# Kernel optimization log

Hardware: AMD Instinct MI355X
Metric: run time of the kernel (lower is better)

## Reference

```python
import jax, jax.numpy as jnp
import numpy as np

# Grid / problem sizes (full-res grid for sp_tensor_1; sp_tensor_2 lives on the half-res grid
# and its indices are multiplied by 2 in forward, so they land on even full-res coords).
B, Z, Y, X = 2, 21, 400, 352
Z2, Y2, X2 = 11, 200, 176
N1, N2 = 160000, 60000
CIN, COUT = 64, 128
EPS = 1e-3  # BatchNorm eps


def _build_rulebook():
    """Precompute the SubMConv3d rulebook (spconv builds this once per indice_key).
    Returns padded gather/scatter index arrays for the 26 non-center taps and N.
    Padding uses index N (a dummy zero row / dropped output row)."""
    rng = np.random.default_rng(0)
    # sp_tensor_2: unique voxels on half-res grid, coords scaled by 2 (as done in forward)
    lin2 = rng.choice(B * Z2 * Y2 * X2, size=N2, replace=False)
    b2 = lin2 // (Z2 * Y2 * X2); r = lin2 % (Z2 * Y2 * X2)
    z2 = r // (Y2 * X2); r = r % (Y2 * X2); y2 = r // X2; x2 = r % X2
    c2 = np.stack([b2, 2 * z2, 2 * y2, 2 * x2], 1).astype(np.int64)
    key2 = ((c2[:, 0] * Z + c2[:, 1]) * Y + c2[:, 2]) * X + c2[:, 3]
    # sp_tensor_1: unique voxels on full-res grid, disjoint from scaled sp2 voxels
    lin1 = rng.choice(B * Z * Y * X, size=N1 + 20000, replace=False)
    lin1 = lin1[~np.isin(lin1, key2)][:N1].astype(np.int64)
    b1 = lin1 // (Z * Y * X); r = lin1 % (Z * Y * X)
    z1 = r // (Y * X); r = r % (Y * X); y1 = r // X; x1 = r % X
    c1 = np.stack([b1, z1, y1, x1], 1)
    coords = np.concatenate([c1, c2], 0)  # [N,4] -- sp1 rows first, matching feature concat
    N = coords.shape[0]
    keys = ((coords[:, 0] * Z + coords[:, 1]) * Y + coords[:, 2]) * X + coords[:, 3]
    order = np.argsort(keys); skeys = keys[order]
    gathers, scatters = [], []
    for dz in (-1, 0, 1):
        for dy in (-1, 0, 1):
            for dx in (-1, 0, 1):
                if dz == 0 and dy == 0 and dx == 0:
                    continue  # center tap handled as a dense identity-indexed GEMM
                q = coords[:, 1:] + np.array([dz, dy, dx])
                valid = (q >= 0).all(1) & (q[:, 0] < Z) & (q[:, 1] < Y) & (q[:, 2] < X)
                qk = ((coords[:, 0] * Z + q[:, 0]) * Y + q[:, 1]) * X + q[:, 2]
                pos = np.clip(np.searchsorted(skeys, qk), 0, N - 1)
                hit = valid & (skeys[pos] == qk)
                gathers.append(order[pos[hit]])
                scatters.append(np.nonzero(hit)[0])
    Pmax = max(len(g) for g in gathers)
    G = np.full((26, Pmax), N, np.int32)
    S = np.full((26, Pmax), N, np.int32)
    for i, (g, s) in enumerate(zip(gathers, scatters)):
        G[i, :len(g)] = g
        S[i, :len(s)] = s
    return G, S, N


def setup_inputs() -> dict:
    G, S, N = _build_rulebook()
    k1, k2, k3, k4 = jax.random.split(jax.random.key(0), 4)
    return {
        "features1": jax.random.normal(k1, (N1, CIN), jnp.float32),
        "features2": jax.random.normal(k2, (N - N1, CIN), jnp.float32),
        "weight": jax.random.normal(k3, (27, CIN, COUT), jnp.float32) * (1.0 / np.sqrt(27 * CIN)),
        "bias": jax.random.normal(k4, (COUT,), jnp.float32) * 0.01,
        "gamma": jnp.ones((COUT,), jnp.float32),
        "beta": jnp.zeros((COUT,), jnp.float32),
        "gather_idx": jnp.asarray(G),
        "scatter_idx": jnp.asarray(S),
    }


def reference(features1, features2, weight, bias, gamma, beta, gather_idx, scatter_idx):
    # forward(): concat features of both sparse tensors along the voxel axis
    feats = jnp.concatenate([features1, features2], axis=0)  # [N, Cin]
    N = feats.shape[0]
    # SubMConv3d via gather-GEMM-scatter over the precomputed rulebook.
    # Center tap (kernel index 13): every output voxel pairs with itself -> dense GEMM.
    out = feats @ weight[13] + bias  # [N, Cout]
    # dummy row N absorbs padded rulebook entries
    out = jnp.concatenate([out, jnp.zeros((1, out.shape[1]), out.dtype)], axis=0)
    feats_pad = jnp.concatenate([feats, jnp.zeros((1, feats.shape[1]), feats.dtype)], axis=0)
    taps = [k for k in range(27) if k != 13]
    for i, k in enumerate(taps):
        msg = feats_pad[gather_idx[i]] @ weight[k]  # [Pmax, Cout]
        out = out.at[scatter_idx[i]].add(msg)
    out = out[:N]
    # BatchNorm1d (training mode: batch statistics, biased variance) + ReLU
    mean = jnp.mean(out, axis=0)
    var = jnp.var(out, axis=0)
    out = (out - mean) * jax.lax.rsqrt(var + EPS) * gamma + beta
    return jax.nn.relu(out)
```

## Files before the change

kernel.cpp:

```cpp
#include <hip/hip_runtime.h>

#define EPS 1e-3f

typedef __attribute__((ext_vector_type(8))) short bf8_t;
typedef __attribute__((ext_vector_type(4))) float f32x4;

static __device__ __forceinline__ unsigned f2bf_pack(float a, float b) {
  union { float f; unsigned u; } ca, cb;
  ca.f = a; cb.f = b;
  unsigned ra = (ca.u + 0x7FFFu + ((ca.u >> 16) & 1u)) >> 16;
  unsigned rb = (cb.u + 0x7FFFu + ((cb.u >> 16) & 1u)) >> 16;
  return ra | (rb << 16);
}
static __device__ __forceinline__ unsigned short f2bf1(float x) {
  union { float f; unsigned u; } c; c.f = x;
  return (unsigned short)((c.u + 0x7FFFu + ((c.u >> 16) & 1u)) >> 16);
}
static __device__ __forceinline__ float bf2f(unsigned bits16) {
  union { unsigned u; float f; } c;
  c.u = bits16 << 16;
  return c.f;
}


__global__ __launch_bounds__(256) void to_bf16(
    const float* __restrict__ f1, const float* __restrict__ f2,
    unsigned short* __restrict__ fbuf, int N1, int N) {
  int idx = blockIdx.x * 256 + threadIdx.x;
  if (idx >= (N + 1) * 8) return;
  int row = idx >> 3, seg = idx & 7;
  uint4 o = make_uint4(0, 0, 0, 0);
  if (row < N) {
    const float* src = (row < N1) ? (f1 + (size_t)row * 64)
                                  : (f2 + (size_t)(row - N1) * 64);
    float4 v0 = *(const float4*)(src + seg * 8);
    float4 v1 = *(const float4*)(src + seg * 8 + 4);
    o.x = f2bf_pack(v0.x, v0.y); o.y = f2bf_pack(v0.z, v0.w);
    o.z = f2bf_pack(v1.x, v1.y); o.w = f2bf_pack(v1.z, v1.w);
  }
  *(uint4*)(fbuf + (size_t)idx * 8) = o;
}

__global__ __launch_bounds__(256) void wconv(
    const float* __restrict__ W, unsigned short* __restrict__ Wb) {
  int idx = blockIdx.x * 256 + threadIdx.x;
  int k = idx & 63, n = (idx >> 6) & 127, t = idx >> 13;
  Wb[idx] = f2bf1(W[((size_t)t * 64 + k) * 128 + n]);
}

__global__ __launch_bounds__(256) void count_slots(
    const int* __restrict__ S, unsigned char* __restrict__ SL,
    int* __restrict__ cnt, int N, int pm) {
  const int p = blockIdx.x * 256 + threadIdx.x;
  const int i = blockIdx.y;
  if (p >= pm) return;
  const int idx = i * pm + p;
  const int s = S[idx];
  if (s < N) SL[idx] = (unsigned char)atomicAdd(&cnt[s], 1);
}

__global__ __launch_bounds__(256) void prefix_base(
    const int* __restrict__ cnt, int2* __restrict__ BC,
    int* __restrict__ gtot, int N) {
  const int t = threadIdx.x;
  const int j0 = blockIdx.x * 1024 + t * 4;
  int c0 = 0, c1 = 0, c2 = 0, c3 = 0;
  if (j0 + 3 < N) {
    int4 c = *(const int4*)(cnt + j0);
    c0 = c.x; c1 = c.y; c2 = c.z; c3 = c.w;
  } else {
    if (j0 < N) c0 = cnt[j0];
    if (j0 + 1 < N) c1 = cnt[j0 + 1];
    if (j0 + 2 < N) c2 = cnt[j0 + 2];
  }
  const int tsum = c0 + c1 + c2 + c3;
  int incl = tsum;
#pragma unroll
  for (int off = 1; off < 64; off <<= 1) {
    int u = __shfl_up(incl, off, 64);
    if ((t & 63) >= off) incl += u;
  }
  __shared__ int wsum[4];
  if ((t & 63) == 63) wsum[t >> 6] = incl;
  __syncthreads();
  if (t == 0) {
    int w0 = wsum[0], w1 = wsum[1], w2 = wsum[2], w3 = wsum[3];
    int gb = atomicAdd(gtot, w0 + w1 + w2 + w3);
    wsum[0] = gb; wsum[1] = gb + w0;
    wsum[2] = gb + w0 + w1; wsum[3] = gb + w0 + w1 + w2;
  }
  __syncthreads();
  const int excl = wsum[t >> 6] + incl - tsum;
  if (j0 < N) BC[j0] = make_int2(excl, c0);
  if (j0 + 1 < N) BC[j0 + 1] = make_int2(excl + c0, c1);
  if (j0 + 2 < N) BC[j0 + 2] = make_int2(excl + c0 + c1, c2);
  if (j0 + 3 < N) BC[j0 + 3] = make_int2(excl + c0 + c1 + c2, c3);
}

__global__ __launch_bounds__(256) void center_mfma(
    const unsigned short* __restrict__ fbuf,
    const unsigned short* __restrict__ Wb13,
    const float* __restrict__ bias,
    unsigned short* __restrict__ outb, int N) {
  __shared__ unsigned short A[128 * 64];
  const int tid = threadIdx.x;
  const int row0 = blockIdx.x * 128;

#pragma unroll
  for (int it = 0; it < 4; ++it) {
    int flat = it * 256 + tid;
    int r = flat >> 3, qs = flat & 7;
    int g = row0 + r; if (g >= N) g = N;
    uint4 v = *(const uint4*)(fbuf + (size_t)g * 64 + qs * 8);
    int rt = r >> 4, m = r & 15, c = qs >> 2, qq = qs & 3;
    *(uint4*)(A + ((rt * 2 + c) * 64 + qq * 16 + m) * 8) = v;
  }
  __syncthreads();

  const int wave = tid >> 6, lane = tid & 63;
  const int ncol = lane & 15, q2 = lane >> 4;
  bf8_t Bf[2][2];
  float bs[2];
#pragma unroll
  for (int ct = 0; ct < 2; ++ct) {
    int col = wave * 32 + ct * 16 + ncol;
    bs[ct] = bias[col];
#pragma unroll
    for (int c = 0; c < 2; ++c)
      Bf[ct][c] = *(const bf8_t*)(Wb13 + (size_t)col * 64 + c * 32 + q2 * 8);
  }
  f32x4 acc[8][2];
#pragma unroll
  for (int rt = 0; rt < 8; ++rt)
#pragma unroll
    for (int ct = 0; ct < 2; ++ct) acc[rt][ct] = (f32x4){0.f, 0.f, 0.f, 0.f};

#pragma unroll
  for (int rt = 0; rt < 8; ++rt) {
    bf8_t a0 = *(const bf8_t*)(A + ((rt * 2 + 0) * 64 + lane) * 8);
    bf8_t a1 = *(const bf8_t*)(A + ((rt * 2 + 1) * 64 + lane) * 8);
#pragma unroll
    for (int ct = 0; ct < 2; ++ct) {
      acc[rt][ct] = __builtin_amdgcn_mfma_f32_16x16x32_bf16(a0, Bf[ct][0], acc[rt][ct], 0, 0, 0);
      acc[rt][ct] = __builtin_amdgcn_mfma_f32_16x16x32_bf16(a1, Bf[ct][1], acc[rt][ct], 0, 0, 0);
    }
  }

#pragma unroll
  for (int rt = 0; rt < 8; ++rt)
#pragma unroll
    for (int ct = 0; ct < 2; ++ct) {
      int col = wave * 32 + ct * 16 + ncol;
#pragma unroll
      for (int e = 0; e < 4; ++e) {
        int row = row0 + rt * 16 + q2 * 4 + e;
        if (row < N)
          outb[(size_t)row * 128 + col] = f2bf1(acc[rt][ct][e] + bs[ct]);
      }
    }
}

__global__ __launch_bounds__(256) void msg_mfma_c(
    const unsigned short* __restrict__ fbuf,
    const unsigned short* __restrict__ Wb,
    const int* __restrict__ G, const int* __restrict__ S,
    const int2* __restrict__ BC, const unsigned char* __restrict__ SL,
    unsigned short* __restrict__ compact, int N, int pm) {
  const int tap = blockIdx.y;
  const int ktap = tap + (tap >= 13 ? 1 : 0);
  const unsigned short* Wt = Wb + (size_t)ktap * 128 * 64;
  const int* Gi = G + (size_t)tap * pm;
  const int* Si = S + (size_t)tap * pm;
  const int p0 = blockIdx.x * 128;
  if (Gi[p0] >= N) return;

  __shared__ unsigned short A[128 * 64];
  __shared__ int g_lds[128];
  __shared__ int d_lds[128];
  const int tid = threadIdx.x;
  if (tid < 128) {
    int p = p0 + tid;
    int g = N, d = -1;
    if (p < pm) {
      g = Gi[p];
      int s = Si[p];
      if (s < N) d = BC[s].x + (int)SL[(size_t)tap * pm + p];
    }
    g_lds[tid] = g;
    d_lds[tid] = d;
  }
  __syncthreads();

#pragma unroll
  for (int it = 0; it < 4; ++it) {
    int flat = it * 256 + tid;
    int r = flat >> 3, qs = flat & 7;
    int g = g_lds[r];
    uint4 v = *(const uint4*)(fbuf + (size_t)g * 64 + qs * 8);
    int rt = r >> 4, m = r & 15, c = qs >> 2, qq = qs & 3;
    *(uint4*)(A + ((rt * 2 + c) * 64 + qq * 16 + m) * 8) = v;
  }
  __syncthreads();

  const int wave = tid >> 6, lane = tid & 63;
  const int ncol = lane & 15, q2 = lane >> 4;
  bf8_t Bf[2][2];
#pragma unroll
  for (int ct = 0; ct < 2; ++ct) {
    int col = wave * 32 + ct * 16 + ncol;
#pragma unroll
    for (int c = 0; c < 2; ++c)
      Bf[ct][c] = *(const bf8_t*)(Wt + (size_t)col * 64 + c * 32 + q2 * 8);
  }
  f32x4 acc[8][2];
#pragma unroll
  for (int rt = 0; rt < 8; ++rt)
#pragma unroll
    for (int ct = 0; ct < 2; ++ct) acc[rt][ct] = (f32x4){0.f, 0.f, 0.f, 0.f};

#pragma unroll
  for (int rt = 0; rt < 8; ++rt) {
    bf8_t a0 = *(const bf8_t*)(A + ((rt * 2 + 0) * 64 + lane) * 8);
    bf8_t a1 = *(const bf8_t*)(A + ((rt * 2 + 1) * 64 + lane) * 8);
#pragma unroll
    for (int ct = 0; ct < 2; ++ct) {
      acc[rt][ct] = __builtin_amdgcn_mfma_f32_16x16x32_bf16(a0, Bf[ct][0], acc[rt][ct], 0, 0, 0);
      acc[rt][ct] = __builtin_amdgcn_mfma_f32_16x16x32_bf16(a1, Bf[ct][1], acc[rt][ct], 0, 0, 0);
    }
  }

#pragma unroll
  for (int rt = 0; rt < 8; ++rt) {
    int dl[4];
#pragma unroll
    for (int e = 0; e < 4; ++e) dl[e] = d_lds[rt * 16 + q2 * 4 + e];
#pragma unroll
    for (int ct = 0; ct < 2; ++ct) {
      int col = wave * 32 + ct * 16 + ncol;
#pragma unroll
      for (int e = 0; e < 4; ++e)
        if (dl[e] >= 0)
          compact[(size_t)dl[e] * 128 + col] = f2bf1(acc[rt][ct][e]);
    }
  }
}

__global__ __launch_bounds__(256) void combine_c(
    unsigned short* __restrict__ outb, const int2* __restrict__ BC,
    const unsigned short* __restrict__ compact, float* __restrict__ ws,
    int N) {
  const int tid = threadIdx.x;
  const int grp = tid >> 5, l = tid & 31;
  float4 s = make_float4(0.f, 0.f, 0.f, 0.f);
  float4 q = make_float4(0.f, 0.f, 0.f, 0.f);

  for (int j = blockIdx.x * 8 + grp; j < N; j += gridDim.x * 8) {
    int2 bc = BC[j];
    uint2 ov = ((const uint2*)(outb + (size_t)j * 128))[l];
    float4 v;
    v.x = bf2f(ov.x & 0xffffu); v.y = bf2f(ov.x >> 16);
    v.z = bf2f(ov.y & 0xffffu); v.w = bf2f(ov.y >> 16);
    for (int k = 0; k < bc.y; ++k) {
      uint2 mv = ((const uint2*)(compact + (size_t)(bc.x + k) * 128))[l];
      v.x += bf2f(mv.x & 0xffffu); v.y += bf2f(mv.x >> 16);
      v.z += bf2f(mv.y & 0xffffu); v.w += bf2f(mv.y >> 16);
    }
    if (bc.y) {
      uint2 pk;
      pk.x = f2bf_pack(v.x, v.y); pk.y = f2bf_pack(v.z, v.w);
      ((uint2*)(outb + (size_t)j * 128))[l] = pk;
    }
    s.x += v.x; s.y += v.y; s.z += v.z; s.w += v.w;
    q.x += v.x * v.x; q.y += v.y * v.y; q.z += v.z * v.z; q.w += v.w * v.w;
  }

  __shared__ float red[8 * 32 * 9];
  float* my = red + (grp * 32 + l) * 9;
  my[0] = s.x; my[1] = s.y; my[2] = s.z; my[3] = s.w;
  my[4] = q.x; my[5] = q.y; my[6] = q.z; my[7] = q.w;
  __syncthreads();
  {
    int c4 = tid & 31, jj = tid >> 5;
    float v = 0.f;
#pragma unroll
    for (int g = 0; g < 8; ++g) v += red[(g * 32 + c4) * 9 + jj];
    int col = c4 * 4 + (jj & 3);
    unsafeAtomicAdd(&ws[(jj >> 2) * 4096 + col * 16], v);
  }
}

__global__ __launch_bounds__(256) void norm_b(
    const unsigned short* __restrict__ outb, float* __restrict__ out,
    const float* __restrict__ ws, const float* __restrict__ gamma,
    const float* __restrict__ beta, int total8, float invN) {
  const int tid0 = blockIdx.x * 256 + threadIdx.x;
  const int c0 = (tid0 & 15) * 8;
  float sc[8], sh[8];
#pragma unroll
  for (int k = 0; k < 8; ++k) {
    float m = ws[(c0 + k) * 16] * invN;
    float var = ws[4096 + (c0 + k) * 16] * invN - m * m;
    sc[k] = gamma[c0 + k] * rsqrtf(var + EPS);
    sh[k] = beta[c0 + k] - m * sc[k];
  }
  for (int idx = tid0; idx < total8; idx += gridDim.x * 256) {
    uint4 v = *(const uint4*)(outb + (size_t)idx * 8);
    float f0 = bf2f(v.x & 0xffffu), f1 = bf2f(v.x >> 16);
    float f2 = bf2f(v.y & 0xffffu), f3 = bf2f(v.y >> 16);
    float f4 = bf2f(v.z & 0xffffu), f5 = bf2f(v.z >> 16);
    float f6 = bf2f(v.w & 0xffffu), f7 = bf2f(v.w >> 16);
    float4 o0, o1;
    o0.x = fmaxf(f0 * sc[0] + sh[0], 0.f);
    o0.y = fmaxf(f1 * sc[1] + sh[1], 0.f);
    o0.z = fmaxf(f2 * sc[2] + sh[2], 0.f);
    o0.w = fmaxf(f3 * sc[3] + sh[3], 0.f);
    o1.x = fmaxf(f4 * sc[4] + sh[4], 0.f);
    o1.y = fmaxf(f5 * sc[5] + sh[5], 0.f);
    o1.z = fmaxf(f6 * sc[6] + sh[6], 0.f);
    o1.w = fmaxf(f7 * sc[7] + sh[7], 0.f);
    *(float4*)(out + (size_t)idx * 8) = o0;
    *(float4*)(out + (size_t)idx * 8 + 4) = o1;
  }
}


__global__ __launch_bounds__(256) void scatter_R(
    const int* __restrict__ S, int* __restrict__ R, int N, int pm) {
  const int p = blockIdx.x * 256 + threadIdx.x;
  const int i = blockIdx.y;
  if (p >= pm) return;
  const int idx = i * pm + p;
  const int s = S[idx];
  if (s < N) R[(size_t)s * 26 + i] = idx;
}

__global__ __launch_bounds__(256) void center_gemm(
    const float* __restrict__ f1, const float* __restrict__ f2,
    const float* __restrict__ W, const float* __restrict__ bias,
    float* __restrict__ out, int N, int N1) {
  __shared__ float fLDS[128 * 65];
  __shared__ float wLDS[32 * 128];
  const int tid = threadIdx.x;
  const int tx = tid & 15, ty = tid >> 4;
  const int row0 = blockIdx.x * 128;

  for (int k = 0; k < 8; ++k) {
    int flat4 = tid + k * 256;
    int row = flat4 >> 4, c4 = flat4 & 15;
    int grow = row0 + row;
    float4 v = make_float4(0.f, 0.f, 0.f, 0.f);
    if (grow < N) {
      const float* src = (grow < N1) ? (f1 + (size_t)grow * 64)
                                     : (f2 + (size_t)(grow - N1) * 64);
      v = *(const float4*)(src + c4 * 4);
    }
    int l = row * 65 + c4 * 4;
    fLDS[l + 0] = v.x; fLDS[l + 1] = v.y; fLDS[l + 2] = v.z; fLDS[l + 3] = v.w;
  }
  float acc[8][8];
#pragma unroll
  for (int r = 0; r < 8; ++r)
#pragma unroll
    for (int j = 0; j < 8; ++j) acc[r][j] = 0.f;
  for (int kk = 0; kk < 64; kk += 32) {
    __syncthreads();
    for (int k = 0; k < 4; ++k) {
      int flat4 = tid + k * 256;
      int c = flat4 >> 5, col4 = flat4 & 31;
      float4 v = *(const float4*)(W + (size_t)(kk + c) * 128 + col4 * 4);
      *(float4*)(wLDS + c * 128 + col4 * 4) = v;
    }
    __syncthreads();
#pragma unroll 4
    for (int c = 0; c < 32; ++c) {
      float a[8];
#pragma unroll
      for (int r = 0; r < 8; ++r) a[r] = fLDS[(ty * 8 + r) * 65 + kk + c];
      float4 b0 = *(const float4*)(wLDS + c * 128 + tx * 8);
      float4 b1 = *(const float4*)(wLDS + c * 128 + tx * 8 + 4);
      float b[8] = {b0.x, b0.y, b0.z, b0.w, b1.x, b1.y, b1.z, b1.w};
#pragma unroll
      for (int r = 0; r < 8; ++r)
#pragma unroll
        for (int j = 0; j < 8; ++j) acc[r][j] += a[r] * b[j];
    }
  }
  float4 bi0 = *(const float4*)(bias + tx * 8);
  float4 bi1 = *(const float4*)(bias + tx * 8 + 4);
#pragma unroll
  for (int r = 0; r < 8; ++r) {
    int grow = row0 + ty * 8 + r;
    if (grow < N) {
      float4 o0 = make_float4(acc[r][0] + bi0.x, acc[r][1] + bi0.y,
                              acc[r][2] + bi0.z, acc[r][3] + bi0.w);
      float4 o1 = make_float4(acc[r][4] + bi1.x, acc[r][5] + bi1.y,
                              acc[r][6] + bi1.z, acc[r][7] + bi1.w);
      float* dst = out + (size_t)grow * 128 + tx * 8;
      *(float4*)dst = o0;
      *(float4*)(dst + 4) = o1;
    }
  }
}

__global__ __launch_bounds__(256) void msg_gemm_buf(
    const float* __restrict__ f1, const float* __restrict__ f2,
    const float* __restrict__ W27, const int* __restrict__ G,
    const int* __restrict__ S, unsigned short* __restrict__ msgbuf,
    int N, int N1, int pm) {
  const int i = blockIdx.y;
  const int ktap = i + (i >= 13 ? 1 : 0);
  const float* W = W27 + (size_t)ktap * 64 * 128;
  const int* Gi = G + (size_t)i * pm;
  const int* Si = S + (size_t)i * pm;
  const int p0 = blockIdx.x * 128;
  if (Si[p0] >= N) return;
  __shared__ float fLDS[128 * 65];
  __shared__ float wLDS[32 * 128];
  const int tid = threadIdx.x;
  const int tx = tid & 15, ty = tid >> 4;
  for (int k = 0; k < 8; ++k) {
    int flat4 = tid + k * 256;
    int row = flat4 >> 4, c4 = flat4 & 15;
    int p = p0 + row;
    float4 v = make_float4(0.f, 0.f, 0.f, 0.f);
    if (p < pm) {
      int g = Gi[p];
      if (g < N) {
        const float* src = (g < N1) ? (f1 + (size_t)g * 64)
                                    : (f2 + (size_t)(g - N1) * 64);
        v = *(const float4*)(src + c4 * 4);
      }
    }
    int l = row * 65 + c4 * 4;
    fLDS[l + 0] = v.x; fLDS[l + 1] = v.y; fLDS[l + 2] = v.z; fLDS[l + 3] = v.w;
  }
  float acc[8][8];
#pragma unroll
  for (int r = 0; r < 8; ++r)
#pragma unroll
    for (int j = 0; j < 8; ++j) acc[r][j] = 0.f;
// ... 82 lines not shown
    __syncthreads();
#pragma unroll 4
    for (int c = 0; c < 32; ++c) {
      float a[8];
#pragma unroll
      for (int r = 0; r < 8; ++r) a[r] = fLDS[(ty * 8 + r) * 65 + kk + c];
      float4 b0 = *(const float4*)(wLDS + c * 128 + tx * 8);
      float4 b1 = *(const float4*)(wLDS + c * 128 + tx * 8 + 4);
      float b[8] = {b0.x, b0.y, b0.z, b0.w, b1.x, b1.y, b1.z, b1.w};
#pragma unroll
      for (int r = 0; r < 8; ++r)
#pragma unroll
        for (int j = 0; j < 8; ++j) acc[r][j] += a[r] * b[j];
    }
  }
#pragma unroll
  for (int r = 0; r < 8; ++r) {
    int p = p0 + ty * 8 + r;
    if (p < pm) {
      int s = Si[p];
      if (s < N) {
        float* dst = out + (size_t)s * 128 + tx * 8;
#pragma unroll
        for (int j = 0; j < 8; ++j) unsafeAtomicAdd(dst + j, acc[r][j]);
      }
    }
  }
}

__global__ __launch_bounds__(256) void combine_stats(
    float* __restrict__ out, const int* __restrict__ R,
    const unsigned short* __restrict__ msgbuf, float* __restrict__ ws,
    int N) {
  const int tid = threadIdx.x;
  const int grp = tid >> 5, l = tid & 31;
  const int base = tid & 32;
  float4 s = make_float4(0.f, 0.f, 0.f, 0.f);
  float4 q = make_float4(0.f, 0.f, 0.f, 0.f);
  for (int j = blockIdx.x * 8 + grp; j < N; j += gridDim.x * 8) {
    float4 v = ((const float4*)(out + (size_t)j * 128))[l];
    int r = (l < 26) ? R[(size_t)j * 26 + l] : -1;
    unsigned long long bal = __ballot(r >= 0);
    unsigned mym = (unsigned)((bal >> base) & 0x3FFFFFFull);
    const bool any = (mym != 0);
    while (mym) {
      int b = __builtin_ctz(mym);
      mym &= mym - 1;
      int ptr = __shfl(r, base + b, 64);
      uint2 mv = ((const uint2*)(msgbuf + (size_t)ptr * 128))[l];
      v.x += bf2f(mv.x & 0xffffu);
      v.y += bf2f(mv.x >> 16);
      v.z += bf2f(mv.y & 0xffffu);
      v.w += bf2f(mv.y >> 16);
    }
    if (any) ((float4*)(out + (size_t)j * 128))[l] = v;
    s.x += v.x; s.y += v.y; s.z += v.z; s.w += v.w;
    q.x += v.x * v.x; q.y += v.y * v.y; q.z += v.z * v.z; q.w += v.w * v.w;
  }
  __shared__ float red[8 * 32 * 8];
  float* my = red + (grp * 32 + l) * 8;
  my[0] = s.x; my[1] = s.y; my[2] = s.z; my[3] = s.w;
  my[4] = q.x; my[5] = q.y; my[6] = q.z; my[7] = q.w;
  __syncthreads();
  {
    int c4 = tid & 31, j = tid >> 5;
    float v = 0.f;
#pragma unroll
    for (int g = 0; g < 8; ++g) v += red[(g * 32 + c4) * 8 + j];
    int col = c4 * 4 + (j & 3);
    unsafeAtomicAdd(&ws[col + (j >> 2) * 128], v);
  }
}

__global__ __launch_bounds__(256) void stats_kernel(
    const float* __restrict__ out, float* __restrict__ ws, int total4) {
  const int tid = threadIdx.x;
  float4 s = make_float4(0.f, 0.f, 0.f, 0.f);
  float4 q = make_float4(0.f, 0.f, 0.f, 0.f);
  const float4* o4 = (const float4*)out;
  for (int idx = blockIdx.x * 256 + tid; idx < total4; idx += gridDim.x * 256) {
    float4 v = o4[idx];
    s.x += v.x; s.y += v.y; s.z += v.z; s.w += v.w;
    q.x += v.x * v.x; q.y += v.y * v.y; q.z += v.z * v.z; q.w += v.w * v.w;
  }
  __shared__ float red[8 * 32 * 8];
  const int col4 = tid & 31, grpq = tid >> 5;
  float* my = red + (grpq * 32 + col4) * 8;
  my[0] = s.x; my[1] = s.y; my[2] = s.z; my[3] = s.w;
  my[4] = q.x; my[5] = q.y; my[6] = q.z; my[7] = q.w;
  __syncthreads();
  {
    int c4 = tid & 31, j = tid >> 5;
    float v = 0.f;
#pragma unroll
    for (int g = 0; g < 8; ++g) v += red[(g * 32 + c4) * 8 + j];
    int col = c4 * 4 + (j & 3);
    unsafeAtomicAdd(&ws[col + (j >> 2) * 128], v);
  }
}

__global__ __launch_bounds__(256) void norm_kernel(
    float* __restrict__ out, const float* __restrict__ ws,
    const float* __restrict__ gamma, const float* __restrict__ beta,
    int total4, float invN) {
  const int tid = threadIdx.x;
  const int c4 = tid & 31;
  float4 s = ((const float4*)ws)[c4];
  float4 q = ((const float4*)ws)[32 + c4];
  float4 g = ((const float4*)gamma)[c4];
  float4 b = ((const float4*)beta)[c4];
  float m0 = s.x * invN, m1 = s.y * invN, m2 = s.z * invN, m3 = s.w * invN;
  float sc0 = g.x * rsqrtf(q.x * invN - m0 * m0 + EPS);
  float sc1 = g.y * rsqrtf(q.y * invN - m1 * m1 + EPS);
  float sc2 = g.z * rsqrtf(q.z * invN - m2 * m2 + EPS);
  float sc3 = g.w * rsqrtf(q.w * invN - m3 * m3 + EPS);
  float sh0 = b.x - m0 * sc0, sh1 = b.y - m1 * sc1;
  float sh2 = b.z - m2 * sc2, sh3 = b.w - m3 * sc3;
  float4* o4 = (float4*)out;
  for (int idx = blockIdx.x * 256 + tid; idx < total4; idx += gridDim.x * 256) {
    float4 v = o4[idx];
    v.x = fmaxf(v.x * sc0 + sh0, 0.f);
    v.y = fmaxf(v.y * sc1 + sh1, 0.f);
    v.z = fmaxf(v.z * sc2 + sh2, 0.f);
    v.w = fmaxf(v.w * sc3 + sh3, 0.f);
    o4[idx] = v;
  }
}

extern "C" void kernel_launch(void* const* d_in, const int* in_sizes, int n_in,
                              void* d_out, int out_size, void* d_ws, size_t ws_size,
                              hipStream_t stream) {
  const float* f1 = (const float*)d_in[0];
  const float* f2 = (const float*)d_in[1];
  const float* W = (const float*)d_in[2];
  const float* bias = (const float*)d_in[3];
  const float* gamma = (const float*)d_in[4];
  const float* beta = (const float*)d_in[5];
  const int* G = (const int*)d_in[6];
  const int* S = (const int*)d_in[7];
  const int N1 = in_sizes[0] / 64;
  const int N2 = in_sizes[1] / 64;
  const int N = N1 + N2;
  const int pm = in_sizes[6] / 26;
  float* out = (float*)d_out;
  float* ws = (float*)d_ws;

  const size_t AL = 255;
  const size_t offC = 32768;
  const size_t Cb = (size_t)N * 4;
  const size_t offBC = (offC + Cb + AL) & ~AL;
  const size_t BCb = (size_t)N * 8;
  const size_t offSL = (offBC + BCb + AL) & ~AL;
  const size_t SLb = (size_t)26 * pm;
  const size_t offF = (offSL + SLb + AL) & ~AL;
  const size_t Fb = (size_t)(N + 1) * 64 * 2;
  const size_t offW = (offF + Fb + AL) & ~AL;
  const size_t Wbyt = (size_t)27 * 128 * 64 * 2;
  const size_t offM = (offW + Wbyt + AL) & ~AL;
  const size_t Mb = (size_t)26 * pm * 128 * 2;
  const size_t offO = (offM + Mb + AL) & ~AL;
  const size_t Ob = (size_t)N * 128 * 2;
  const bool full = ws_size >= offO + Ob;

  const size_t Rb = (size_t)N * 26 * 4;
  const size_t offR2 = 1024;
  const size_t offM2 = (offR2 + Rb + AL) & ~AL;
  const bool fast2 = ws_size >= offM2 + Mb;

  if (full) {
    int* cnt = (int*)((char*)d_ws + offC);
    int2* BC = (int2*)((char*)d_ws + offBC);
    unsigned char* SLp = (unsigned char*)((char*)d_ws + offSL);
    unsigned short* fbuf = (unsigned short*)((char*)d_ws + offF);
    unsigned short* Wb = (unsigned short*)((char*)d_ws + offW);
    unsigned short* compact = (unsigned short*)((char*)d_ws + offM);
    unsigned short* outb = (unsigned short*)((char*)d_ws + offO);
    int* gtot = (int*)((char*)d_ws + 28672);

    (void)hipMemsetAsync(ws, 0, 32768, stream);
    (void)hipMemsetAsync(cnt, 0, Cb, stream);
    to_bf16<<<((N + 1) * 8 + 255) / 256, 256, 0, stream>>>(f1, f2, fbuf, N1, N);
    wconv<<<(27 * 128 * 64) / 256, 256, 0, stream>>>(W, Wb);
    count_slots<<<dim3((pm + 255) / 256, 26), 256, 0, stream>>>(S, SLp, cnt, N, pm);
    prefix_base<<<(N + 1023) / 1024, 256, 0, stream>>>(cnt, BC, gtot, N);

    center_mfma<<<(N + 127) / 128, 256, 0, stream>>>(
        fbuf, Wb + (size_t)13 * 128 * 64, bias, outb, N);
    msg_mfma_c<<<dim3((pm + 127) / 128, 26), 256, 0, stream>>>(
        fbuf, Wb, G, S, BC, SLp, compact, N, pm);

    combine_c<<<2048, 256, 0, stream>>>(outb, BC, compact, ws, N);
    norm_b<<<2048, 256, 0, stream>>>(outb, out, ws, gamma, beta, N * 16,
                                     1.0f / N);
  } else if (fast2) {
    int* R = (int*)((char*)d_ws + offR2);
    unsigned short* msgbuf = (unsigned short*)((char*)d_ws + offM2);
    (void)hipMemsetAsync(ws, 0, 256 * sizeof(float), stream);
    (void)hipMemsetAsync(R, 0xFF, Rb, stream);
    center_gemm<<<(N + 127) / 128, 256, 0, stream>>>(
        f1, f2, W + (size_t)13 * 64 * 128, bias, out, N, N1);
    scatter_R<<<dim3((pm + 255) / 256, 26), 256, 0, stream>>>(S, R, N, pm);
    msg_gemm_buf<<<dim3((pm + 127) / 128, 26), 256, 0, stream>>>(
        f1, f2, W, G, S, msgbuf, N, N1, pm);
    combine_stats<<<1024, 256, 0, stream>>>(out, R, msgbuf, ws, N);
    norm_kernel<<<2048, 256, 0, stream>>>(out, ws, gamma, beta, N * 32,
                                          1.0f / N);
  } else {
    (void)hipMemsetAsync(ws, 0, 256 * sizeof(float), stream);
    center_gemm<<<(N + 127) / 128, 256, 0, stream>>>(
        f1, f2, W + (size_t)13 * 64 * 128, bias, out, N, N1);
    msg_gemm<<<dim3((pm + 127) / 128, 26), 256, 0, stream>>>(
        f1, f2, W, G, S, out, N, N1, pm);
    stats_kernel<<<1024, 256, 0, stream>>>(out, ws, N * 32);
    norm_kernel<<<2048, 256, 0, stream>>>(out, ws, gamma, beta, N * 32,
                                          1.0f / N);
  }
}
```

Baseline: 334.1 us.

## Fuse bf16 conversion into GEMMs and center GEMM into combine

Removes the separate fp32-to-bf16 feature buffer, so the message and center GEMM kernels read fp32 features directly and convert while staging into LDS. The center GEMM is fused with the combine/statistics pass, so output rows are written once after adding the compacted messages. Weight conversion and slot counting are merged into one launch, and the two memsets become one. This cuts launches and a full round trip of the bf16 feature and output buffers. In exchange, gathers now read twice as many bytes of fp32 per row, and the combine's compact reads are per-column scalar loads rather than vectorised.

```diff
diff --git a/kernel.cpp b/kernel.cpp
--- a/kernel.cpp
+++ b/kernel.cpp
@@ -23,40 +23,24 @@
 }
 
 
-__global__ __launch_bounds__(256) void to_bf16(
-    const float* __restrict__ f1, const float* __restrict__ f2,
-    unsigned short* __restrict__ fbuf, int N1, int N) {
-  int idx = blockIdx.x * 256 + threadIdx.x;
-  if (idx >= (N + 1) * 8) return;
-  int row = idx >> 3, seg = idx & 7;
-  uint4 o = make_uint4(0, 0, 0, 0);
-  if (row < N) {
-    const float* src = (row < N1) ? (f1 + (size_t)row * 64)
-                                  : (f2 + (size_t)(row - N1) * 64);
-    float4 v0 = *(const float4*)(src + seg * 8);
-    float4 v1 = *(const float4*)(src + seg * 8 + 4);
-    o.x = f2bf_pack(v0.x, v0.y); o.y = f2bf_pack(v0.z, v0.w);
-    o.z = f2bf_pack(v1.x, v1.y); o.w = f2bf_pack(v1.z, v1.w);
-  }
-  *(uint4*)(fbuf + (size_t)idx * 8) = o;
-}
-
-__global__ __launch_bounds__(256) void wconv(
-    const float* __restrict__ W, unsigned short* __restrict__ Wb) {
-  int idx = blockIdx.x * 256 + threadIdx.x;
-  int k = idx & 63, n = (idx >> 6) & 127, t = idx >> 13;
-  Wb[idx] = f2bf1(W[((size_t)t * 64 + k) * 128 + n]);
-}
-
-__global__ __launch_bounds__(256) void count_slots(
+__global__ __launch_bounds__(256) void prep(
+    const float* __restrict__ W, unsigned short* __restrict__ Wb,
     const int* __restrict__ S, unsigned char* __restrict__ SL,
-    int* __restrict__ cnt, int N, int pm) {
-  const int p = blockIdx.x * 256 + threadIdx.x;
-  const int i = blockIdx.y;
-  if (p >= pm) return;
-  const int idx = i * pm + p;
-  const int s = S[idx];
-  if (s < N) SL[idx] = (unsigned char)atomicAdd(&cnt[s], 1);
+    int* __restrict__ cnt, int N, int pm, int wblocks, int cpb) {
+  const int bid = blockIdx.x;
+  if (bid < wblocks) {
+    int idx = bid * 256 + threadIdx.x;
+    int k = idx & 63, n = (idx >> 6) & 127, t = idx >> 13;
+    Wb[idx] = f2bf1(W[((size_t)t * 64 + k) * 128 + n]);
+  } else {
+    int b = bid - wblocks;
+    int tap = b / cpb;
+    int p = (b - tap * cpb) * 256 + threadIdx.x;
+    if (p >= pm) return;
+    const int idx = tap * pm + p;
+    const int s = S[idx];
+    if (s < N) SL[idx] = (unsigned char)atomicAdd(&cnt[s], 1);
+  }
 }
 
 __global__ __launch_bounds__(256) void prefix_base(
@@ -97,75 +81,12 @@
   if (j0 + 3 < N) BC[j0 + 3] = make_int2(excl + c0 + c1 + c2, c3);
 }
 
-__global__ __launch_bounds__(256) void center_mfma(
-    const unsigned short* __restrict__ fbuf,
-    const unsigned short* __restrict__ Wb13,
-    const float* __restrict__ bias,
-    unsigned short* __restrict__ outb, int N) {
-  __shared__ unsigned short A[128 * 64];
-  const int tid = threadIdx.x;
-  const int row0 = blockIdx.x * 128;
-
-#pragma unroll
-  for (int it = 0; it < 4; ++it) {
-    int flat = it * 256 + tid;
-    int r = flat >> 3, qs = flat & 7;
-    int g = row0 + r; if (g >= N) g = N;
-    uint4 v = *(const uint4*)(fbuf + (size_t)g * 64 + qs * 8);
-    int rt = r >> 4, m = r & 15, c = qs >> 2, qq = qs & 3;
-    *(uint4*)(A + ((rt * 2 + c) * 64 + qq * 16 + m) * 8) = v;
-  }
-  __syncthreads();
-
-  const int wave = tid >> 6, lane = tid & 63;
-  const int ncol = lane & 15, q2 = lane >> 4;
-  bf8_t Bf[2][2];
-  float bs[2];
-#pragma unroll
-  for (int ct = 0; ct < 2; ++ct) {
-    int col = wave * 32 + ct * 16 + ncol;
-    bs[ct] = bias[col];
-#pragma unroll
-    for (int c = 0; c < 2; ++c)
-      Bf[ct][c] = *(const bf8_t*)(Wb13 + (size_t)col * 64 + c * 32 + q2 * 8);
-  }
-  f32x4 acc[8][2];
-#pragma unroll
-  for (int rt = 0; rt < 8; ++rt)
-#pragma unroll
-    for (int ct = 0; ct < 2; ++ct) acc[rt][ct] = (f32x4){0.f, 0.f, 0.f, 0.f};
-
-#pragma unroll
-  for (int rt = 0; rt < 8; ++rt) {
-    bf8_t a0 = *(const bf8_t*)(A + ((rt * 2 + 0) * 64 + lane) * 8);
-    bf8_t a1 = *(const bf8_t*)(A + ((rt * 2 + 1) * 64 + lane) * 8);
-#pragma unroll
-    for (int ct = 0; ct < 2; ++ct) {
-      acc[rt][ct] = __builtin_amdgcn_mfma_f32_16x16x32_bf16(a0, Bf[ct][0], acc[rt][ct], 0, 0, 0);
-      acc[rt][ct] = __builtin_amdgcn_mfma_f32_16x16x32_bf16(a1, Bf[ct][1], acc[rt][ct], 0, 0, 0);
-    }
-  }
-
-#pragma unroll
-  for (int rt = 0; rt < 8; ++rt)
-#pragma unroll
-    for (int ct = 0; ct < 2; ++ct) {
-      int col = wave * 32 + ct * 16 + ncol;
-#pragma unroll
-      for (int e = 0; e < 4; ++e) {
-        int row = row0 + rt * 16 + q2 * 4 + e;
-        if (row < N)
-          outb[(size_t)row * 128 + col] = f2bf1(acc[rt][ct][e] + bs[ct]);
-      }
-    }
-}
-
 __global__ __launch_bounds__(256) void msg_mfma_c(
-    const unsigned short* __restrict__ fbuf,
+    const float* __restrict__ f1, const float* __restrict__ f2,
     const unsigned short* __restrict__ Wb,
     const int* __restrict__ G, const int* __restrict__ S,
     const int2* __restrict__ BC, const unsigned char* __restrict__ SL,
-    unsigned short* __restrict__ compact, int N, int pm) {
+    unsigned short* __restrict__ compact, int N, int N1, int pm) {
   const int tap = blockIdx.y;
   const int ktap = tap + (tap >= 13 ? 1 : 0);
   const unsigned short* Wt = Wb + (size_t)ktap * 128 * 64;
@@ -196,9 +117,17 @@
     int flat = it * 256 + tid;
     int r = flat >> 3, qs = flat & 7;
     int g = g_lds[r];
-    uint4 v = *(const uint4*)(fbuf + (size_t)g * 64 + qs * 8);
+    uint4 o = make_uint4(0, 0, 0, 0);
+    if (g < N) {
+      const float* src = (g < N1) ? (f1 + (size_t)g * 64)
+                                  : (f2 + (size_t)(g - N1) * 64);
+      float4 v0 = *(const float4*)(src + qs * 8);
+      float4 v1 = *(const float4*)(src + qs * 8 + 4);
+      o.x = f2bf_pack(v0.x, v0.y); o.y = f2bf_pack(v0.z, v0.w);
+      o.z = f2bf_pack(v1.x, v1.y); o.w = f2bf_pack(v1.z, v1.w);
+    }
     int rt = r >> 4, m = r & 15, c = qs >> 2, qq = qs & 3;
-    *(uint4*)(A + ((rt * 2 + c) * 64 + qq * 16 + m) * 8) = v;
+    *(uint4*)(A + ((rt * 2 + c) * 64 + qq * 16 + m) * 8) = o;
   }
   __syncthreads();
 
@@ -245,47 +174,108 @@
   }
 }
 
-__global__ __launch_bounds__(256) void combine_c(
-    unsigned short* __restrict__ outb, const int2* __restrict__ BC,
-    const unsigned short* __restrict__ compact, float* __restrict__ ws,
-    int N) {
+__global__ __launch_bounds__(256) void center_combine(
+    const float* __restrict__ f1, const float* __restrict__ f2,
+    const unsigned short* __restrict__ Wb13, const float* __restrict__ bias,
+    const int2* __restrict__ BC, const unsigned short* __restrict__ compact,
+    unsigned short* __restrict__ outb, float* __restrict__ ws,
+    int N, int N1) {
+  __shared__ unsigned short A[128 * 64];
+  __shared__ int2 bc_lds[128];
+  __shared__ float2 red2[128 * 4];
   const int tid = threadIdx.x;
-  const int grp = tid >> 5, l = tid & 31;
-  float4 s = make_float4(0.f, 0.f, 0.f, 0.f);
-  float4 q = make_float4(0.f, 0.f, 0.f, 0.f);
-
-  for (int j = blockIdx.x * 8 + grp; j < N; j += gridDim.x * 8) {
-    int2 bc = BC[j];
-    uint2 ov = ((const uint2*)(outb + (size_t)j * 128))[l];
-    float4 v;
-    v.x = bf2f(ov.x & 0xffffu); v.y = bf2f(ov.x >> 16);
-    v.z = bf2f(ov.y & 0xffffu); v.w = bf2f(ov.y >> 16);
-    for (int k = 0; k < bc.y; ++k) {
-      uint2 mv = ((const uint2*)(compact + (size_t)(bc.x + k) * 128))[l];
-      v.x += bf2f(mv.x & 0xffffu); v.y += bf2f(mv.x >> 16);
-      v.z += bf2f(mv.y & 0xffffu); v.w += bf2f(mv.y >> 16);
-    }
-    if (bc.y) {
-      uint2 pk;
-      pk.x = f2bf_pack(v.x, v.y); pk.y = f2bf_pack(v.z, v.w);
-      ((uint2*)(outb + (size_t)j * 128))[l] = pk;
-    }
-    s.x += v.x; s.y += v.y; s.z += v.z; s.w += v.w;
-    q.x += v.x * v.x; q.y += v.y * v.y; q.z += v.z * v.z; q.w += v.w * v.w;
-  }
-
-  __shared__ float red[8 * 32 * 9];
-  float* my = red + (grp * 32 + l) * 9;
-  my[0] = s.x; my[1] = s.y; my[2] = s.z; my[3] = s.w;
-  my[4] = q.x; my[5] = q.y; my[6] = q.z; my[7] = q.w;
+  const int row0 = blockIdx.x * 128;
+
+  if (tid < 128) {
+    int r = row0 + tid;
+    int2 bc = make_int2(0, 0);
+    if (r < N) bc = BC[r];
+    bc_lds[tid] = bc;
+  }
+
+#pragma unroll
+  for (int it = 0; it < 4; ++it) {
+    int flat = it * 256 + tid;
+    int r = flat >> 3, qs = flat & 7;
+    int g = row0 + r;
+    uint4 o = make_uint4(0, 0, 0, 0);
+    if (g < N) {
+      const float* src = (g < N1) ? (f1 + (size_t)g * 64)
+                                  : (f2 + (size_t)(g - N1) * 64);
+      float4 v0 = *(const float4*)(src + qs * 8);
+      float4 v1 = *(const float4*)(src + qs * 8 + 4);
+      o.x = f2bf_pack(v0.x, v0.y); o.y = f2bf_pack(v0.z, v0.w);
+      o.z = f2bf_pack(v1.x, v1.y); o.w = f2bf_pack(v1.z, v1.w);
+    }
+    int rt = r >> 4, m = r & 15, c = qs >> 2, qq = qs & 3;
+    *(uint4*)(A + ((rt * 2 + c) * 64 + qq * 16 + m) * 8) = o;
+  }
   __syncthreads();
-  {
-    int c4 = tid & 31, jj = tid >> 5;
-    float v = 0.f;
-#pragma unroll
-    for (int g = 0; g < 8; ++g) v += red[(g * 32 + c4) * 9 + jj];
-    int col = c4 * 4 + (jj & 3);
-    unsafeAtomicAdd(&ws[(jj >> 2) * 4096 + col * 16], v);
+
+  const int wave = tid >> 6, lane = tid & 63;
+  const int ncol = lane & 15, q2 = lane >> 4;
+  bf8_t Bf[2][2];
+  float bs[2];
+#pragma unroll
+  for (int ct = 0; ct < 2; ++ct) {
+    int col = wave * 32 + ct * 16 + ncol;
+    bs[ct] = bias[col];
+#pragma unroll
+    for (int c = 0; c < 2; ++c)
+      Bf[ct][c] = *(const bf8_t*)(Wb13 + (size_t)col * 64 + c * 32 + q2 * 8);
+  }
+  f32x4 acc[8][2];
+#pragma unroll
+  for (int rt = 0; rt < 8; ++rt)
+#pragma unroll
+    for (int ct = 0; ct < 2; ++ct) acc[rt][ct] = (f32x4){0.f, 0.f, 0.f, 0.f};
+
+#pragma unroll
+  for (int rt = 0; rt < 8; ++rt) {
+    bf8_t a0 = *(const bf8_t*)(A + ((rt * 2 + 0) * 64 + lane) * 8);
+    bf8_t a1 = *(const bf8_t*)(A + ((rt * 2 + 1) * 64 + lane) * 8);
+#pragma unroll
+    for (int ct = 0; ct < 2; ++ct) {
+      acc[rt][ct] = __builtin_amdgcn_mfma_f32_16x16x32_bf16(a0, Bf[ct][0], acc[rt][ct], 0, 0, 0);
+      acc[rt][ct] = __builtin_amdgcn_mfma_f32_16x16x32_bf16(a1, Bf[ct][1], acc[rt][ct], 0, 0, 0);
+    }
+  }
+
+  float sacc[2] = {0.f, 0.f}, qacc[2] = {0.f, 0.f};
+#pragma unroll
+  for (int rt = 0; rt < 8; ++rt) {
+    int2 bcv[4];
+#pragma unroll
+    for (int e = 0; e < 4; ++e) bcv[e] = bc_lds[rt * 16 + q2 * 4 + e];
+#pragma unroll
+    for (int ct = 0; ct < 2; ++ct) {
+      int col = wave * 32 + ct * 16 + ncol;
+#pragma unroll
+      for (int e = 0; e < 4; ++e) {
+        int row = row0 + rt * 16 + q2 * 4 + e;
+        if (row < N) {
+          float v = acc[rt][ct][e] + bs[ct];
+          for (int k = 0; k < bcv[e].y; ++k)
+            v += bf2f(compact[(size_t)(bcv[e].x + k) * 128 + col]);
+          outb[(size_t)row * 128 + col] = f2bf1(v);
+          sacc[ct] += v; qacc[ct] += v * v;
+        }
+      }
+    }
+  }
+#pragma unroll
+  for (int ct = 0; ct < 2; ++ct) {
+    int col = wave * 32 + ct * 16 + ncol;
+    red2[col * 4 + q2] = make_float2(sacc[ct], qacc[ct]);
+  }
+  __syncthreads();
+  if (tid < 128) {
+    float2 a0 = red2[tid * 4 + 0], a1 = red2[tid * 4 + 1];
+    float2 a2 = red2[tid * 4 + 2], a3 = red2[tid * 4 + 3];
+    float ssum = a0.x + a1.x + a2.x + a3.x;
+    float qsum = a0.y + a1.y + a2.y + a3.y;
+    unsafeAtomicAdd(&ws[tid * 16], ssum);
+    unsafeAtomicAdd(&ws[4096 + tid * 16], qsum);
   }
 }
 
@@ -674,9 +664,7 @@
   const size_t BCb = (size_t)N * 8;
   const size_t offSL = (offBC + BCb + AL) & ~AL;
   const size_t SLb = (size_t)26 * pm;
-  const size_t offF = (offSL + SLb + AL) & ~AL;
-  const size_t Fb = (size_t)(N + 1) * 64 * 2;
-  const size_t offW = (offF + Fb + AL) & ~AL;
+  const size_t offW = (offSL + SLb + AL) & ~AL;
   const size_t Wbyt = (size_t)27 * 128 * 64 * 2;
   const size_t offM = (offW + Wbyt + AL) & ~AL;
   const size_t Mb = (size_t)26 * pm * 128 * 2;
@@ -693,25 +681,23 @@
     int* cnt = (int*)((char*)d_ws + offC);
     int2* BC = (int2*)((char*)d_ws + offBC);
     unsigned char* SLp = (unsigned char*)((char*)d_ws + offSL);
-    unsigned short* fbuf = (unsigned short*)((char*)d_ws + offF);
     unsigned short* Wb = (unsigned short*)((char*)d_ws + offW);
     unsigned short* compact = (unsigned short*)((char*)d_ws + offM);
     unsigned short* outb = (unsigned short*)((char*)d_ws + offO);
     int* gtot = (int*)((char*)d_ws + 28672);
 
-    (void)hipMemsetAsync(ws, 0, 32768, stream);
-    (void)hipMemsetAsync(cnt, 0, Cb, stream);
-    to_bf16<<<((N + 1) * 8 + 255) / 256, 256, 0, stream>>>(f1, f2, fbuf, N1, N);
-    wconv<<<(27 * 128 * 64) / 256, 256, 0, stream>>>(W, Wb);
-    count_slots<<<dim3((pm + 255) / 256, 26), 256, 0, stream>>>(S, SLp, cnt, N, pm);
+    const int wblocks = (27 * 128 * 64) / 256;
+    const int cpb = (pm + 255) / 256;
+
+    (void)hipMemsetAsync(ws, 0, offC + Cb, stream);
+    prep<<<wblocks + 26 * cpb, 256, 0, stream>>>(W, Wb, S, SLp, cnt, N, pm,
+                                                 wblocks, cpb);
     prefix_base<<<(N + 1023) / 1024, 256, 0, stream>>>(cnt, BC, gtot, N);
-
-    center_mfma<<<(N + 127) / 128, 256, 0, stream>>>(
-        fbuf, Wb + (size_t)13 * 128 * 64, bias, outb, N);
     msg_mfma_c<<<dim3((pm + 127) / 128, 26), 256, 0, stream>>>(
-        fbuf, Wb, G, S, BC, SLp, compact, N, pm);
-
-    combine_c<<<2048, 256, 0, stream>>>(outb, BC, compact, ws, N);
+        f1, f2, Wb, G, S, BC, SLp, compact, N, N1, pm);
+    center_combine<<<(N + 127) / 128, 256, 0, stream>>>(
+        f1, f2, Wb + (size_t)13 * 128 * 64, bias, BC, compact, outb, ws,
+        N, N1);
     norm_b<<<2048, 256, 0, stream>>>(outb, out, ws, gamma, beta, N * 16,
                                      1.0f / N);
   } else if (fast2) {
```

Result: slower. 353.1 us (+5.7%).

## Fuse feature conversion into conv GEMM and merge prep and center kernels

Applied to the files above, without the earlier changes.

Removes the separate bf16 feature conversion pass; the conv kernel now gathers fp32 features directly and converts them while staging into LDS. Weight conversion and slot counting are merged into one prep kernel, the center and message GEMMs into one launch, and the two memsets into one. This cuts launches and the fbuf write/read round trip, but doubles the gather bytes per row (fp32 instead of bf16) for the 26 tap gathers.

```diff
diff --git a/kernel.cpp b/kernel.cpp
--- a/kernel.cpp
+++ b/kernel.cpp
@@ -23,40 +23,24 @@
 }
 
 
-__global__ __launch_bounds__(256) void to_bf16(
-    const float* __restrict__ f1, const float* __restrict__ f2,
-    unsigned short* __restrict__ fbuf, int N1, int N) {
-  int idx = blockIdx.x * 256 + threadIdx.x;
-  if (idx >= (N + 1) * 8) return;
-  int row = idx >> 3, seg = idx & 7;
-  uint4 o = make_uint4(0, 0, 0, 0);
-  if (row < N) {
-    const float* src = (row < N1) ? (f1 + (size_t)row * 64)
-                                  : (f2 + (size_t)(row - N1) * 64);
-    float4 v0 = *(const float4*)(src + seg * 8);
-    float4 v1 = *(const float4*)(src + seg * 8 + 4);
-    o.x = f2bf_pack(v0.x, v0.y); o.y = f2bf_pack(v0.z, v0.w);
-    o.z = f2bf_pack(v1.x, v1.y); o.w = f2bf_pack(v1.z, v1.w);
-  }
-  *(uint4*)(fbuf + (size_t)idx * 8) = o;
-}
-
-__global__ __launch_bounds__(256) void wconv(
-    const float* __restrict__ W, unsigned short* __restrict__ Wb) {
-  int idx = blockIdx.x * 256 + threadIdx.x;
-  int k = idx & 63, n = (idx >> 6) & 127, t = idx >> 13;
-  Wb[idx] = f2bf1(W[((size_t)t * 64 + k) * 128 + n]);
-}
-
-__global__ __launch_bounds__(256) void count_slots(
+__global__ __launch_bounds__(256) void prep(
+    const float* __restrict__ W, unsigned short* __restrict__ Wb,
     const int* __restrict__ S, unsigned char* __restrict__ SL,
-    int* __restrict__ cnt, int N, int pm) {
-  const int p = blockIdx.x * 256 + threadIdx.x;
-  const int i = blockIdx.y;
-  if (p >= pm) return;
-  const int idx = i * pm + p;
-  const int s = S[idx];
-  if (s < N) SL[idx] = (unsigned char)atomicAdd(&cnt[s], 1);
+    int* __restrict__ cnt, int N, int pm, int wblocks, int cpb) {
+  const int bid = blockIdx.x;
+  if (bid < wblocks) {
+    int idx = bid * 256 + threadIdx.x;
+    int k = idx & 63, n = (idx >> 6) & 127, t = idx >> 13;
+    Wb[idx] = f2bf1(W[((size_t)t * 64 + k) * 128 + n]);
+  } else {
+    int b = bid - wblocks;
+    int tap = b / cpb;
+    int p = (b - tap * cpb) * 256 + threadIdx.x;
+    if (p >= pm) return;
+    const int idx = tap * pm + p;
+    const int s = S[idx];
+    if (s < N) SL[idx] = (unsigned char)atomicAdd(&cnt[s], 1);
+  }
 }
 
 __global__ __launch_bounds__(256) void prefix_base(
@@ -97,97 +81,46 @@
   if (j0 + 3 < N) BC[j0 + 3] = make_int2(excl + c0 + c1 + c2, c3);
 }
 
-__global__ __launch_bounds__(256) void center_mfma(
-    const unsigned short* __restrict__ fbuf,
-    const unsigned short* __restrict__ Wb13,
-    const float* __restrict__ bias,
-    unsigned short* __restrict__ outb, int N) {
-  __shared__ unsigned short A[128 * 64];
-  const int tid = threadIdx.x;
-  const int row0 = blockIdx.x * 128;
-
-#pragma unroll
-  for (int it = 0; it < 4; ++it) {
-    int flat = it * 256 + tid;
-    int r = flat >> 3, qs = flat & 7;
-    int g = row0 + r; if (g >= N) g = N;
-    uint4 v = *(const uint4*)(fbuf + (size_t)g * 64 + qs * 8);
-    int rt = r >> 4, m = r & 15, c = qs >> 2, qq = qs & 3;
-    *(uint4*)(A + ((rt * 2 + c) * 64 + qq * 16 + m) * 8) = v;
-  }
-  __syncthreads();
-
-  const int wave = tid >> 6, lane = tid & 63;
-  const int ncol = lane & 15, q2 = lane >> 4;
-  bf8_t Bf[2][2];
-  float bs[2];
-#pragma unroll
-  for (int ct = 0; ct < 2; ++ct) {
-    int col = wave * 32 + ct * 16 + ncol;
-    bs[ct] = bias[col];
-#pragma unroll
-    for (int c = 0; c < 2; ++c)
-      Bf[ct][c] = *(const bf8_t*)(Wb13 + (size_t)col * 64 + c * 32 + q2 * 8);
-  }
-  f32x4 acc[8][2];
-#pragma unroll
-  for (int rt = 0; rt < 8; ++rt)
-#pragma unroll
-    for (int ct = 0; ct < 2; ++ct) acc[rt][ct] = (f32x4){0.f, 0.f, 0.f, 0.f};
-
-#pragma unroll
-  for (int rt = 0; rt < 8; ++rt) {
-    bf8_t a0 = *(const bf8_t*)(A + ((rt * 2 + 0) * 64 + lane) * 8);
-    bf8_t a1 = *(const bf8_t*)(A + ((rt * 2 + 1) * 64 + lane) * 8);
-#pragma unroll
-    for (int ct = 0; ct < 2; ++ct) {
-      acc[rt][ct] = __builtin_amdgcn_mfma_f32_16x16x32_bf16(a0, Bf[ct][0], acc[rt][ct], 0, 0, 0);
-      acc[rt][ct] = __builtin_amdgcn_mfma_f32_16x16x32_bf16(a1, Bf[ct][1], acc[rt][ct], 0, 0, 0);
-    }
-  }
-
-#pragma unroll
-  for (int rt = 0; rt < 8; ++rt)
-#pragma unroll
-    for (int ct = 0; ct < 2; ++ct) {
-      int col = wave * 32 + ct * 16 + ncol;
-#pragma unroll
-      for (int e = 0; e < 4; ++e) {
-        int row = row0 + rt * 16 + q2 * 4 + e;
-        if (row < N)
-          outb[(size_t)row * 128 + col] = f2bf1(acc[rt][ct][e] + bs[ct]);
-      }
-    }
-}
-
-__global__ __launch_bounds__(256) void msg_mfma_c(
-    const unsigned short* __restrict__ fbuf,
-    const unsigned short* __restrict__ Wb,
+__global__ __launch_bounds__(256) void conv_mfma(
+    const float* __restrict__ f1, const float* __restrict__ f2,
+    const unsigned short* __restrict__ Wb, const float* __restrict__ bias,
     const int* __restrict__ G, const int* __restrict__ S,
     const int2* __restrict__ BC, const unsigned char* __restrict__ SL,
-    unsigned short* __restrict__ compact, int N, int pm) {
-  const int tap = blockIdx.y;
-  const int ktap = tap + (tap >= 13 ? 1 : 0);
-  const unsigned short* Wt = Wb + (size_t)ktap * 128 * 64;
-  const int* Gi = G + (size_t)tap * pm;
-  const int* Si = S + (size_t)tap * pm;
-  const int p0 = blockIdx.x * 128;
-  if (Gi[p0] >= N) return;
-
+    unsigned short* __restrict__ compact, unsigned short* __restrict__ outb,
+    int N, int N1, int pm, int cblocks, int cpb) {
   __shared__ unsigned short A[128 * 64];
   __shared__ int g_lds[128];
   __shared__ int d_lds[128];
   const int tid = threadIdx.x;
-  if (tid < 128) {
-    int p = p0 + tid;
-    int g = N, d = -1;
-    if (p < pm) {
-      g = Gi[p];
-      int s = Si[p];
-      if (s < N) d = BC[s].x + (int)SL[(size_t)tap * pm + p];
-    }
-    g_lds[tid] = g;
-    d_lds[tid] = d;
+  const int bid = blockIdx.x;
+  const bool is_center = (bid < cblocks);
+  const unsigned short* Wt;
+  int row0 = 0;
+
+  if (is_center) {
+    row0 = bid * 128;
+    Wt = Wb + (size_t)13 * 128 * 64;
+    if (tid < 128) g_lds[tid] = row0 + tid;
+  } else {
+    const int b = bid - cblocks;
+    const int tap = b / cpb;
+    const int p0 = (b - tap * cpb) * 128;
+    const int* Gi = G + (size_t)tap * pm;
+    if (Gi[p0] >= N) return;
+    const int ktap = tap + (tap >= 13 ? 1 : 0);
+    Wt = Wb + (size_t)ktap * 128 * 64;
+    const int* Si = S + (size_t)tap * pm;
+    if (tid < 128) {
+      int p = p0 + tid;
+      int g = N, d = -1;
+      if (p < pm) {
+        g = Gi[p];
+        int s = Si[p];
+        if (s < N) d = BC[s].x + (int)SL[(size_t)tap * pm + p];
+      }
+      g_lds[tid] = g;
+      d_lds[tid] = d;
+    }
   }
   __syncthreads();
 
@@ -196,18 +129,28 @@
     int flat = it * 256 + tid;
     int r = flat >> 3, qs = flat & 7;
     int g = g_lds[r];
-    uint4 v = *(const uint4*)(fbuf + (size_t)g * 64 + qs * 8);
+    uint4 o = make_uint4(0, 0, 0, 0);
+    if (g < N) {
+      const float* src = (g < N1) ? (f1 + (size_t)g * 64)
+                                  : (f2 + (size_t)(g - N1) * 64);
+      float4 v0 = *(const float4*)(src + qs * 8);
+      float4 v1 = *(const float4*)(src + qs * 8 + 4);
+      o.x = f2bf_pack(v0.x, v0.y); o.y = f2bf_pack(v0.z, v0.w);
+      o.z = f2bf_pack(v1.x, v1.y); o.w = f2bf_pack(v1.z, v1.w);
+    }
     int rt = r >> 4, m = r & 15, c = qs >> 2, qq = qs & 3;
-    *(uint4*)(A + ((rt * 2 + c) * 64 + qq * 16 + m) * 8) = v;
+    *(uint4*)(A + ((rt * 2 + c) * 64 + qq * 16 + m) * 8) = o;
   }
   __syncthreads();
 
   const int wave = tid >> 6, lane = tid & 63;
   const int ncol = lane & 15, q2 = lane >> 4;
   bf8_t Bf[2][2];
+  float bs[2] = {0.f, 0.f};
 #pragma unroll
   for (int ct = 0; ct < 2; ++ct) {
     int col = wave * 32 + ct * 16 + ncol;
+    if (is_center) bs[ct] = bias[col];
 #pragma unroll
     for (int c = 0; c < 2; ++c)
       Bf[ct][c] = *(const bf8_t*)(Wt + (size_t)col * 64 + c * 32 + q2 * 8);
@@ -229,18 +172,33 @@
     }
   }
 
-#pragma unroll
-  for (int rt = 0; rt < 8; ++rt) {
-    int dl[4];
-#pragma unroll
-    for (int e = 0; e < 4; ++e) dl[e] = d_lds[rt * 16 + q2 * 4 + e];
-#pragma unroll
-    for (int ct = 0; ct < 2; ++ct) {
-      int col = wave * 32 + ct * 16 + ncol;
-#pragma unroll
-      for (int e = 0; e < 4; ++e)
-        if (dl[e] >= 0)
-          compact[(size_t)dl[e] * 128 + col] = f2bf1(acc[rt][ct][e]);
+  if (is_center) {
+#pragma unroll
+    for (int rt = 0; rt < 8; ++rt)
+#pragma unroll
+      for (int ct = 0; ct < 2; ++ct) {
+        int col = wave * 32 + ct * 16 + ncol;
+#pragma unroll
+        for (int e = 0; e < 4; ++e) {
+          int row = row0 + rt * 16 + q2 * 4 + e;
+          if (row < N)
+            outb[(size_t)row * 128 + col] = f2bf1(acc[rt][ct][e] + bs[ct]);
+        }
+      }
+  } else {
+#pragma unroll
+    for (int rt = 0; rt < 8; ++rt) {
+      int dl[4];
+#pragma unroll
+      for (int e = 0; e < 4; ++e) dl[e] = d_lds[rt * 16 + q2 * 4 + e];
+#pragma unroll
+      for (int ct = 0; ct < 2; ++ct) {
+        int col = wave * 32 + ct * 16 + ncol;
+#pragma unroll
+        for (int e = 0; e < 4; ++e)
+          if (dl[e] >= 0)
+            compact[(size_t)dl[e] * 128 + col] = f2bf1(acc[rt][ct][e]);
+      }
     }
   }
 }
@@ -674,9 +632,7 @@
   const size_t BCb = (size_t)N * 8;
   const size_t offSL = (offBC + BCb + AL) & ~AL;
   const size_t SLb = (size_t)26 * pm;
-  const size_t offF = (offSL + SLb + AL) & ~AL;
-  const size_t Fb = (size_t)(N + 1) * 64 * 2;
-  const size_t offW = (offF + Fb + AL) & ~AL;
+  const size_t offW = (offSL + SLb + AL) & ~AL;
   const size_t Wbyt = (size_t)27 * 128 * 64 * 2;
   const size_t offM = (offW + Wbyt + AL) & ~AL;
   const size_t Mb = (size_t)26 * pm * 128 * 2;
@@ -693,24 +649,23 @@
     int* cnt = (int*)((char*)d_ws + offC);
     int2* BC = (int2*)((char*)d_ws + offBC);
     unsigned char* SLp = (unsigned char*)((char*)d_ws + offSL);
-    unsigned short* fbuf = (unsigned short*)((char*)d_ws + offF);
     unsigned short* Wb = (unsigned short*)((char*)d_ws + offW);
     unsigned short* compact = (unsigned short*)((char*)d_ws + offM);
     unsigned short* outb = (unsigned short*)((char*)d_ws + offO);
     int* gtot = (int*)((char*)d_ws + 28672);
 
-    (void)hipMemsetAsync(ws, 0, 32768, stream);
-    (void)hipMemsetAsync(cnt, 0, Cb, stream);
-    to_bf16<<<((N + 1) * 8 + 255) / 256, 256, 0, stream>>>(f1, f2, fbuf, N1, N);
-    wconv<<<(27 * 128 * 64) / 256, 256, 0, stream>>>(W, Wb);
-    count_slots<<<dim3((pm + 255) / 256, 26), 256, 0, stream>>>(S, SLp, cnt, N, pm);
+    const int wblocks = (27 * 128 * 64) / 256;
+    const int cpb256 = (pm + 255) / 256;
+    const int cpb128 = (pm + 127) / 128;
+    const int cblocks = (N + 127) / 128;
+
+    (void)hipMemsetAsync(ws, 0, offC + Cb, stream);
+    prep<<<wblocks + 26 * cpb256, 256, 0, stream>>>(W, Wb, S, SLp, cnt, N, pm,
+                                                    wblocks, cpb256);
     prefix_base<<<(N + 1023) / 1024, 256, 0, stream>>>(cnt, BC, gtot, N);
-
-    center_mfma<<<(N + 127) / 128, 256, 0, stream>>>(
-        fbuf, Wb + (size_t)13 * 128 * 64, bias, outb, N);
-    msg_mfma_c<<<dim3((pm + 127) / 128, 26), 256, 0, stream>>>(
-        fbuf, Wb, G, S, BC, SLp, compact, N, pm);
-
+    conv_mfma<<<cblocks + 26 * cpb128, 256, 0, stream>>>(
+        f1, f2, Wb, bias, G, S, BC, SLp, compact, outb, N, N1, pm,
+        cblocks, cpb128);
     combine_c<<<2048, 256, 0, stream>>>(outb, BC, compact, ws, N);
     norm_b<<<2048, 256, 0, stream>>>(outb, out, ws, gamma, beta, N * 16,
                                      1.0f / N);
```

Measured after the change: 308.8 us. -7.6%, faster.
